# Performance work log

Hardware: AMD Instinct MI355X
Metric: run time of the kernel (lower is better)

The kernel has to match this reference:

```python
import jax, jax.numpy as jnp
import numpy as np

N, E, F_IN, H, O = 50000, 800000, 128, 8, 8  # nodes, edges, in_feat, heads, out-per-head
NEG_SLOPE = 0.2

def setup_inputs() -> dict:
    key = jax.random.key(0)
    k1, k2, k3, k4, k5, k6 = jax.random.split(key, 6)
    h = jax.random.normal(k1, (N, F_IN), dtype=jnp.float32)
    # xavier_uniform-like scale (gain=1.414) expressed via normal init scale
    w_scale = 1.414 * np.sqrt(2.0 / (F_IN + O)).astype(np.float32)
    W = jax.random.normal(k2, (H, F_IN, O), dtype=jnp.float32) * w_scale
    a_scale = 1.414 * np.sqrt(2.0 / (2 * O + 1)).astype(np.float32)
    a1 = jax.random.normal(k3, (H, O), dtype=jnp.float32) * a_scale
    a2 = jax.random.normal(k4, (H, O), dtype=jnp.float32) * a_scale
    src = jax.random.randint(k5, (E,), 0, N, dtype=jnp.int64 if jax.config.jax_enable_x64 else jnp.int32)
    dst = jax.random.randint(k6, (E,), 0, N, dtype=jnp.int64 if jax.config.jax_enable_x64 else jnp.int32)
    return {"h": h, "W": W, "a1": a1, "a2": a2, "src": src, "dst": dst}

def reference(h, W, a1, a2, src, dst):
    # Per-head linear projection: [N, H, O]
    Wh = jnp.einsum('nf,hfo->nho', h, W)
    # Per-node attention half-scores (a split into src/dst halves): [N, H]
    s_src = jnp.einsum('nho,ho->nh', Wh, a1)
    s_dst = jnp.einsum('nho,ho->nh', Wh, a2)
    # Edge attention logits: [E, H]
    e = jax.nn.leaky_relu(s_src[src] + s_dst[dst], negative_slope=NEG_SLOPE)
    # Numerically-stable segment softmax over incoming edges of each dst node
    m = jax.ops.segment_max(e, dst, num_segments=N)          # [N, H]
    m = jnp.where(jnp.isfinite(m), m, jnp.float32(0.0))      # isolated nodes -> 0
    p = jnp.exp(e - m[dst])                                   # [E, H]
    denom = jax.ops.segment_sum(p, dst, num_segments=N)       # [N, H]
    attn = p / jnp.maximum(denom[dst], jnp.float32(1e-16))    # [E, H]
    # Weighted scatter-sum of messages: [N, H, O]
    out = jax.ops.segment_sum(attn[:, :, None] * Wh[src], dst, num_segments=N)
    # Concatenate heads: [N, H*O]
    return out.reshape(N, H * O)
```

## Files before the change

### kernel.cpp

```cpp
#include <hip/hip_runtime.h>
#include <hip/hip_bf16.h>
#include <hip/hip_fp16.h>


#define FIN 128
#define NH 8
#define NO 8
#define NC 64
#define NB_COLS 80
#define GR 64
#define EPB 4096
#define BCAP 8192

typedef __attribute__((ext_vector_type(8))) short bf16x8;
typedef __attribute__((ext_vector_type(4))) float f32x4;

static __device__ __forceinline__ unsigned short f2bf(float f) {
    unsigned u = __float_as_uint(f);
    u += 0x7fff + ((u >> 16) & 1);
    return (unsigned short)(u >> 16);
}

__global__ __launch_bounds__(256) void prep_kernel(
    const float* __restrict__ W, const float* __restrict__ a1, const float* __restrict__ a2,
    unsigned short* __restrict__ wBg, int* __restrict__ bcnt)
{
    const int t = threadIdx.x;
    bcnt[t] = 0;
    for (int i = t; i < NH * FIN * NO; i += 256) {
        int hh = i >> 10, f = (i >> 3) & 127, o = i & 7;
        int c = hh * 8 + o;
        wBg[c * FIN + (f ^ ((c & 7) << 3))] = f2bf(W[i]);
    }
    for (int i = t; i < 16 * FIN; i += 256) {
        int j = i >> 7;
        int f = i & 127;
        int hh = j & 7;
        const float* av = (j < 8) ? (a1 + hh * NO) : (a2 + hh * NO);
        const float* wv = W + hh * (FIN * NO) + f * NO;
        float s = 0.f;
#pragma unroll
        for (int o = 0; o < 8; ++o) s += wv[o] * av[o];
        int c = 64 + j;
        wBg[c * FIN + (f ^ ((c & 7) << 3))] = f2bf(s);
    }
}

__global__ __launch_bounds__(256) void gemm_s_scat_kernel(
    const float* __restrict__ h, const unsigned short* __restrict__ wBg,
    const int* __restrict__ src, const int* __restrict__ dst,
    int* __restrict__ bcnt, unsigned* __restrict__ packed,
    __half* __restrict__ Wh, float* __restrict__ s_src, float* __restrict__ s_dst,
    int N, int E, int gemm_blocks)
{
    __shared__ alignas(16) unsigned short wB[NB_COLS * FIN];
    __shared__ int cnt_l[256];
    __shared__ int base_l[256];
    const int tid = threadIdx.x;

    if (blockIdx.x >= gemm_blocks) {
        const long e0 = (long)(blockIdx.x - gemm_blocks) * EPB;
        cnt_l[tid] = 0;
        __syncthreads();
        int br[16];
        unsigned pk[16];
#pragma unroll
        for (int j = 0; j < 16; ++j) {
            long e = e0 + j * 256 + tid;
            bool ok = (e < E);
            int d = ok ? dst[e] : 0;
            int s = ok ? src[e] : 0;
            int b = d >> 8;
            int r = ok ? atomicAdd(&cnt_l[b], 1) : 0;
            br[j] = ok ? ((b << 16) | r) : -1;
            pk[j] = ((unsigned)(d & 255) << 16) | (unsigned)s;
        }
        __syncthreads();
        if (cnt_l[tid] > 0) base_l[tid] = atomicAdd(&bcnt[tid], cnt_l[tid]);
        __syncthreads();
#pragma unroll
        for (int j = 0; j < 16; ++j) {
            if (br[j] >= 0) {
                int b = br[j] >> 16, r = br[j] & 0xFFFF;
                packed[(long)b * BCAP + base_l[b] + r] = pk[j];
            }
        }
        return;
    }

    const int w    = tid >> 6;
    const int lane = tid & 63;
    const int l15  = lane & 15;
    const int lg   = lane >> 4;

    const int row  = blockIdx.x * GR + w * 16 + l15;
    const int rowc = (row < N) ? row : (N - 1);
    const float* hrow = h + (long)rowc * FIN + lg * 8;
    float4 va[8];
#pragma unroll
    for (int kk = 0; kk < 4; ++kk) {
        va[2 * kk]     = *(const float4*)(hrow + kk * 32);
        va[2 * kk + 1] = *(const float4*)(hrow + kk * 32 + 4);
    }

    {
        const uint4* s4 = (const uint4*)wBg;
        uint4* d4 = (uint4*)wB;
#pragma unroll
        for (int j = 0; j < 5; ++j)
            d4[j * 256 + tid] = s4[j * 256 + tid];
    }
    __syncthreads();

    bf16x8 af[4];
#pragma unroll
    for (int kk = 0; kk < 4; ++kk) {
        bf16x8 r;
        r[0] = (short)f2bf(va[2 * kk].x);     r[1] = (short)f2bf(va[2 * kk].y);
        r[2] = (short)f2bf(va[2 * kk].z);     r[3] = (short)f2bf(va[2 * kk].w);
        r[4] = (short)f2bf(va[2 * kk + 1].x); r[5] = (short)f2bf(va[2 * kk + 1].y);
        r[6] = (short)f2bf(va[2 * kk + 1].z); r[7] = (short)f2bf(va[2 * kk + 1].w);
        af[kk] = r;
    }

    f32x4 acc[5] = {{0,0,0,0},{0,0,0,0},{0,0,0,0},{0,0,0,0},{0,0,0,0}};
#pragma unroll
    for (int kk = 0; kk < 4; ++kk) {
        int kb = kk * 64 + lg * 16;
#pragma unroll
        for (int nt = 0; nt < 5; ++nt) {
            int c = nt * 16 + l15;
            bf16x8 bf = *(const bf16x8*)((const char*)wB + c * (FIN * 2) + (kb ^ ((c & 7) << 4)));
            acc[nt] = __builtin_amdgcn_mfma_f32_16x16x32_bf16(af[kk], bf, acc[nt], 0, 0, 0);
        }
    }

    const int row0 = blockIdx.x * GR;
#pragma unroll
    for (int nt = 0; nt < 4; ++nt) {
        int col = nt * 16 + l15;
#pragma unroll
        for (int r = 0; r < 4; ++r) {
            int n = row0 + w * 16 + lg * 4 + r;
            if (n < N) Wh[(long)n * NC + col] = __float2half_rn(acc[nt][r]);
        }
    }
#pragma unroll
    for (int r = 0; r < 4; ++r) {
        int n = row0 + w * 16 + lg * 4 + r;
        if (n < N) {
            float v = acc[4][r];
            if (l15 < 8) s_src[n * NH + l15] = v;
            else         s_dst[n * NH + (l15 - 8)] = v;
        }
    }
}

__global__ __launch_bounds__(1024) void bucketB_kernel(
    const unsigned* __restrict__ packed, const int* __restrict__ bcnt,
    int* __restrict__ row_off, unsigned short* __restrict__ srcs,
    int N, int E, int nb)
{
    __shared__ int bins[256];
    __shared__ int scan_s[256];
    __shared__ int g0s;
    __shared__ unsigned short outb[BCAP];
    const int t = threadIdx.x;
    const int b = blockIdx.x;
    const int d0 = b << 8;
    const unsigned* pin = packed + (long)b * BCAP;

    int v2 = 0;
    if (t < 256) {
        v2 = (t < nb) ? bcnt[t] : 0;
        scan_s[t] = v2;
        bins[t] = 0;
    }
    __syncthreads();
    for (int off = 1; off < 256; off <<= 1) {
        int u = (t < 256 && t >= off) ? scan_s[t - off] : 0;
        __syncthreads();
        if (t < 256) scan_s[t] += u;
        __syncthreads();
    }
    if (t == b) g0s = scan_s[t] - v2;
    __syncthreads();
    const int g0 = g0s;
    const int cnt = bcnt[b];

    for (int i = t; i < cnt; i += 1024)
        atomicAdd(&bins[pin[i] >> 16], 1);
    __syncthreads();
    int v = 0;
    if (t < 256) { v = bins[t]; scan_s[t] = v; }
    __syncthreads();
    for (int off = 1; off < 256; off <<= 1) {
        int u = (t < 256 && t >= off) ? scan_s[t - off] : 0;
        __syncthreads();
        if (t < 256) scan_s[t] += u;
        __syncthreads();
    }
    if (t < 256) {
        if (d0 + t < N) row_off[d0 + t] = g0 + scan_s[t] - v;
        bins[t] = scan_s[t] - v;
    }
    if (b == nb - 1 && t == 0) row_off[N] = E;
    __syncthreads();
    for (int i = t; i < cnt; i += 1024) {
        unsigned p = pin[i];
        int pos = atomicAdd(&bins[p >> 16], 1);
        outb[pos] = (unsigned short)(p & 0xFFFF);
    }
    __syncthreads();
    for (int i = t; i < cnt; i += 1024)
        srcs[g0 + i] = outb[i];
}

__global__ __launch_bounds__(256) void gather_kernel(
    const unsigned short* __restrict__ srcs, const int* __restrict__ row_off,
    const float* __restrict__ s_src, const float* __restrict__ s_dst,
    const __half* __restrict__ Wh, float* __restrict__ out, int N)
{
    int wid = blockIdx.x * 4 + (threadIdx.x >> 6);
    if (wid >= N) return;
    const int lane = threadIdx.x & 63;
    const int el = lane >> 3;
    const int hh = lane & 7;
    int beg = row_off[wid];
    int end = row_off[wid + 1];
    float sd = s_dst[wid * NH + hh];
    float acc = 0.f, den = 0.f;

    int idx0 = beg + el;
    bool val = (idx0 < end);
    int s = (int)srcs[val ? idx0 : beg];
    float ss = s_src[s * NH + hh];

    for (int i = beg; i < end; i += 8) {
        int ni = i + 8;
        int nidx = ni + el;
        bool nval = (nidx < end);
        int ns = (int)srcs[(ni < end && nval) ? nidx : beg];
        float nss = s_src[ns * NH + hh];
        float x = ss + sd;
        x = (x > 0.f) ? x : 0.2f * x;
        float p = __expf(x);
        p = val ? p : 0.f;
        den += p;
#pragma unroll
        for (int k = 0; k < 8; ++k) {
            int sk   = __shfl(s, k * 8);
            float pk = __shfl(p, k * 8 + el);
            float wv = __half2float(Wh[((unsigned)sk << 6) | (unsigned)lane]);
            acc = fmaf(pk, wv, acc);
        }
        s = ns; ss = nss; val = nval;
    }
    den += __shfl_xor(den, 8);
    den += __shfl_xor(den, 16);
    den += __shfl_xor(den, 32);
    float den_b = __shfl(den, el);
    out[(unsigned)wid * NC + (unsigned)lane] = acc / fmaxf(den_b, 1e-16f);
}

extern "C" void kernel_launch(void* const* d_in, const int* in_sizes, int n_in,
                              void* d_out, int out_size, void* d_ws, size_t ws_size,
                              hipStream_t stream)
{
    const float* h  = (const float*)d_in[0];
    const float* W  = (const float*)d_in[1];
    const float* a1 = (const float*)d_in[2];
    const float* a2 = (const float*)d_in[3];
    const int*  src = (const int*)d_in[4];
    const int*  dst = (const int*)d_in[5];
    float* out = (float*)d_out;

    const int N = in_sizes[0] / FIN;
    const int E = in_sizes[4];
    const int nb = (N + 255) >> 8;

    char* wsb = (char*)d_ws;
    __half* Wh         = (__half*)wsb;           wsb += (size_t)N * NC * 2;
    float* s_src       = (float*)wsb;            wsb += (size_t)N * NH * 4;
    float* s_dst       = (float*)wsb;            wsb += (size_t)N * NH * 4;
    int* row_off       = (int*)wsb;              wsb += (size_t)(N + 1) * 4;
    int* bcnt          = (int*)wsb;              wsb += (size_t)256 * 4;
    unsigned short* wBg = (unsigned short*)wsb;  wsb += (size_t)NB_COLS * FIN * 2;
    unsigned* packed   = (unsigned*)wsb;         wsb += (size_t)nb * BCAP * 4;
    unsigned short* srcs = (unsigned short*)wsb; wsb += (size_t)E * 2;

    prep_kernel<<<1, 256, 0, stream>>>(W, a1, a2, wBg, bcnt);

    const int gemm_blocks = (N + GR - 1) / GR;
    const int scat_blocks = (E + EPB - 1) / EPB;
    gemm_s_scat_kernel<<<gemm_blocks + scat_blocks, 256, 0, stream>>>(
        h, wBg, src, dst, bcnt, packed, Wh, s_src, s_dst, N, E, gemm_blocks);

    bucketB_kernel<<<nb, 1024, 0, stream>>>(packed, bcnt, row_off, srcs, N, E, nb);

    int g_blocks = (N + 3) / 4;
    gather_kernel<<<g_blocks, 256, 0, stream>>>(srcs, row_off, s_src, s_dst, Wh, out, N);
}
```

Measured before the change: 66.90 us.

## Process two destination nodes per wavefront in gather with half2 loads

The gather kernel now splits each 64-lane wavefront into two 32-lane halves, each handling one destination node and four edges per iteration. Each lane loads a packed half2 pair of Wh values and keeps two accumulators, then writes a float2 output. The goal is to avoid wasted lanes on low-degree nodes (average degree is about 16) and to issue wider memory accesses. The cost is loop divergence between the two halves when their nodes have different degrees.

```diff
diff --git a/kernel.cpp b/kernel.cpp
--- a/kernel.cpp
+++ b/kernel.cpp
@@ -221,26 +221,32 @@
     const float* __restrict__ s_src, const float* __restrict__ s_dst,
     const __half* __restrict__ Wh, float* __restrict__ out, int N)
 {
-    int wid = blockIdx.x * 4 + (threadIdx.x >> 6);
-    if (wid >= N) return;
+    const int w    = threadIdx.x >> 6;
     const int lane = threadIdx.x & 63;
-    const int el = lane >> 3;
-    const int hh = lane & 7;
-    int beg = row_off[wid];
-    int end = row_off[wid + 1];
-    float sd = s_dst[wid * NH + hh];
-    float acc = 0.f, den = 0.f;
+    const int half = lane >> 5;
+    const int hb   = half << 5;
+    const int ll   = lane & 31;
+    const int el   = ll >> 3;
+    const int hh   = ll & 7;
+    const int q    = ll >> 2;
+    const int node = blockIdx.x * 8 + w * 2 + half;
+    const bool nvalid = (node < N);
+
+    int beg = nvalid ? row_off[node] : 0;
+    int end = nvalid ? row_off[node + 1] : 0;
+    float sd = nvalid ? s_dst[node * NH + hh] : 0.f;
+    float acc0 = 0.f, acc1 = 0.f, den = 0.f;
 
     int idx0 = beg + el;
     bool val = (idx0 < end);
     int s = (int)srcs[val ? idx0 : beg];
     float ss = s_src[s * NH + hh];
 
-    for (int i = beg; i < end; i += 8) {
-        int ni = i + 8;
-        int nidx = ni + el;
+    const unsigned* Wh32 = (const unsigned*)Wh;
+    for (int i = beg; i < end; i += 4) {
+        int nidx = i + 4 + el;
         bool nval = (nidx < end);
-        int ns = (int)srcs[(ni < end && nval) ? nidx : beg];
+        int ns = (int)srcs[nval ? nidx : beg];
         float nss = s_src[ns * NH + hh];
         float x = ss + sd;
         x = (x > 0.f) ? x : 0.2f * x;
@@ -248,19 +254,24 @@
         p = val ? p : 0.f;
         den += p;
 #pragma unroll
-        for (int k = 0; k < 8; ++k) {
-            int sk   = __shfl(s, k * 8);
-            float pk = __shfl(p, k * 8 + el);
-            float wv = __half2float(Wh[((unsigned)sk << 6) | (unsigned)lane]);
-            acc = fmaf(pk, wv, acc);
+        for (int k = 0; k < 4; ++k) {
+            int sk   = __shfl(s, hb + k * 8);
+            float pk = __shfl(p, hb + k * 8 + q);
+            unsigned wu = Wh32[((unsigned)sk << 5) + ll];
+            float2 wf = __half22float2(*(__half2*)&wu);
+            acc0 = fmaf(pk, wf.x, acc0);
+            acc1 = fmaf(pk, wf.y, acc1);
         }
         s = ns; ss = nss; val = nval;
     }
     den += __shfl_xor(den, 8);
     den += __shfl_xor(den, 16);
-    den += __shfl_xor(den, 32);
-    float den_b = __shfl(den, el);
-    out[(unsigned)wid * NC + (unsigned)lane] = acc / fmaxf(den_b, 1e-16f);
+    float den_b = __shfl(den, hb + q);
+    if (nvalid) {
+        float r = 1.f / fmaxf(den_b, 1e-16f);
+        float2 o; o.x = acc0 * r; o.y = acc1 * r;
+        ((float2*)out)[((unsigned)node << 5) + ll] = o;
+    }
 }
 
 extern "C" void kernel_launch(void* const* d_in, const int* in_sizes, int n_in,
@@ -298,6 +309,6 @@
 
     bucketB_kernel<<<nb, 1024, 0, stream>>>(packed, bcnt, row_off, srcs, N, E, nb);
 
-    int g_blocks = (N + 3) / 4;
+    int g_blocks = (N + 7) / 8;
     gather_kernel<<<g_blocks, 256, 0, stream>>>(srcs, row_off, s_src, s_dst, Wh, out, N);
 }
```

New measurement: 62.13 us. 1.08x faster.
